# Kernel optimization log

Measured on AMD Instinct MI355X. Metric: run time of the kernel, lower is better.

The kernel has to match this reference:

```python
import jax, jax.numpy as jnp
import numpy as np
from jax import lax

# problem sizes and solver hyperparameters
B, N, G, T = 8, 128, 100, 24
N_ITERS, LR, RHO = 40, 2e-4, 10.0
VOLL, VOSP = 1000.0, 50.0
RES_UP, RES_DN, RT_UP, RT_DN, RAMP_F = 0.05, 0.02, 2.0, 0.5, 1.0


def setup_inputs() -> dict:
    k = jax.random.split(jax.random.key(0), 8)
    pmin = jax.random.uniform(k[0], (G,), minval=10.0, maxval=50.0)
    pmax = pmin + jax.random.uniform(k[1], (G,), minval=100.0, maxval=300.0)
    b_G = jax.random.uniform(k[2], (G,), minval=10.0, maxval=40.0)
    c_G = jax.random.uniform(k[3], (G,), minval=0.0, maxval=5.0)
    lo, hi = pmin.sum(), pmax.sum()
    forecast = lo + jax.random.uniform(k[4], (B, T)) * 0.5 * (hi - lo)
    omega_scen = 0.05 * hi * jax.random.normal(k[5], (B, N, T))
    om_min = omega_scen.min(axis=1) - 1.0
    om_max = omega_scen.max(axis=1) + 1.0
    eps = jax.random.uniform(k[6], (B,)) * 5.0
    return dict(forecast=forecast, omega_scen=omega_scen, om_min=om_min,
                om_max=om_max, eps=eps, pmin=pmin, pmax=pmax, b_G=b_G, c_G=c_G)


def _solve_one(forecast, omega, om_min, om_max, eps, pmin, pmax, b, c):
    # forecast [T], omega [N,T], om_min/om_max [T], eps scalar
    ramp = pmax * RAMP_F
    rup_p, rdn_p = RES_UP * b, RES_DN * b
    rtu_p, rtd_p = RT_UP * b, RT_DN * b
    dist_max = (om_max[None, :] - omega).sum(-1)   # [N]
    dist_min = (omega - om_min[None, :]).sum(-1)   # [N]

    def objective(v):
        Cost = b[:, None] * v['P'] + c[:, None]
        stage1 = (Cost.sum() + (rup_p[:, None] * v['R_up']).sum()
                  + (rdn_p[:, None] * v['R_dn']).sum())
        Qn = (jnp.einsum('g,ngt->n', rtu_p, v['d_up'])
              + jnp.einsum('g,ngt->n', rtd_p, v['d_dn'])
              + VOLL * v['LS'].sum(-1) + VOSP * v['SP'].sum(-1))
        Qmax = ((rtu_p[:, None] * v['du_max']).sum() + (rtd_p[:, None] * v['dd_max']).sum()
                + VOLL * v['LS_max'].sum() + VOSP * v['SP_max'].sum())
        Qmin = ((rtu_p[:, None] * v['du_min']).sum() + (rtd_p[:, None] * v['dd_min']).sum()
                + VOLL * v['LS_min'].sum() + VOSP * v['SP_min'].sum())
        # epigraph phi[n] >= Qn, >= Qmax - gamma*dist_max, >= Qmin - gamma*dist_min
        phi = jnp.maximum(Qn, jnp.maximum(Qmax - v['gamma'] * dist_max,
                                          Qmin - v['gamma'] * dist_min))
        obj = stage1 + phi.mean() + eps * v['gamma']
        return obj, (phi, Cost)

    def penalty(v):
        relu = jax.nn.relu
        dP = v['P'][:, 1:] - v['P'][:, :-1]
        res = [
            # equality constraints
            v['P'].sum(0) - forecast,
            (v['d_up'] - v['d_dn']).sum(1) + v['LS'] - v['SP'] - omega,
            (v['du_max'] - v['dd_max']).sum(0) + v['LS_max'] - v['SP_max'] - om_max,
            (v['du_min'] - v['dd_min']).sum(0) + v['LS_min'] - v['SP_min'] - om_min,
            # inequality constraints (relu of violation)
            relu(v['P'] + v['R_up'] - pmax[:, None]),
            relu(pmin[:, None] - (v['P'] - v['R_dn'])),
            relu(v['d_up'] - v['R_up'][None]),
            relu(v['d_dn'] - v['R_dn'][None]),
            relu(v['du_max'] - v['R_up']), relu(v['dd_max'] - v['R_dn']),
            relu(v['du_min'] - v['R_up']), relu(v['dd_min'] - v['R_dn']),
            relu(jnp.abs(dP) - ramp[:, None]),
        ]
        total = jnp.zeros(())
        for r in res:
            total = total + (r * r).sum()
        return total

    def loss(v):
        return objective(v)[0] + RHO * penalty(v)

    def project(v):
        v = {kk: jnp.maximum(vv, 0.0) for kk, vv in v.items()}
        v['P'] = jnp.clip(v['P'], pmin[:, None], pmax[:, None])
        return v

    z_gt = jnp.zeros((G, T))
    v0 = {'P': jnp.broadcast_to(0.5 * (pmin + pmax)[:, None], (G, T)),
          'R_up': z_gt, 'R_dn': z_gt,
          'd_up': jnp.zeros((N, G, T)), 'd_dn': jnp.zeros((N, G, T)),
          'LS': jnp.zeros((N, T)), 'SP': jnp.zeros((N, T)),
          'du_max': z_gt, 'dd_max': z_gt,
          'LS_max': jnp.zeros((T,)), 'SP_max': jnp.zeros((T,)),
          'du_min': z_gt, 'dd_min': z_gt,
          'LS_min': jnp.zeros((T,)), 'SP_min': jnp.zeros((T,)),
          'gamma': jnp.zeros(())}
    grad_fn = jax.grad(loss)

    def step(v, _):
        g = grad_fn(v)
        v = jax.tree_util.tree_map(lambda x, gx: x - LR * gx, v, g)
        return project(v), None

    v, _ = lax.scan(step, v0, None, length=N_ITERS)
    obj, (phi, Cost) = objective(v)
    return v['P'], v['R_up'], v['R_dn'], Cost, phi, v['gamma'], obj


def reference(forecast, omega_scen, om_min, om_max, eps, pmin, pmax, b_G, c_G):
    solve = jax.vmap(_solve_one, in_axes=(0, 0, 0, 0, 0, None, None, None, None))
    P, R_up, R_dn, Cost, phi, gamma, obj = solve(
        forecast, omega_scen, om_min, om_max, eps, pmin, pmax, b_G, c_G)
    return P, R_up, R_dn, Cost, phi, gamma, obj
```

## Files before the change

kernel.cpp:

```cpp
#include <hip/hip_runtime.h>
#include <hip/hip_cooperative_groups.h>

namespace cg = cooperative_groups;

#define G_ 100
#define T_ 24
#define NSC 128
#define BATCH 8
#define NITER 40
#define NBLK (BATCH*T_)
#define NTHR 512
#define GMAX 15

typedef unsigned long long u64;

__device__ __forceinline__ u64 gload64(const u64* p){
  return __hip_atomic_load(p, __ATOMIC_RELAXED, __HIP_MEMORY_SCOPE_AGENT);
}
__device__ __forceinline__ void gstore64(u64* p, u64 v){
  __hip_atomic_store(p, v, __ATOMIC_RELAXED, __HIP_MEMORY_SCOPE_AGENT);
}
__device__ __forceinline__ u64 pack(float v, unsigned tag){
  return ((u64)tag<<32) | (u64)__float_as_uint(v);
}
__device__ __forceinline__ float unpackv(u64 x){ return __uint_as_float((unsigned)x); }
__device__ __forceinline__ unsigned unpackt(u64 x){ return (unsigned)(x>>32); }

__device__ __forceinline__ void blockReduce2(float& a, float& b, float* sR){
#pragma unroll
  for (int off=32; off; off>>=1){ a+=__shfl_down(a,off,64); b+=__shfl_down(b,off,64); }
  const int w = threadIdx.x>>6;
  __syncthreads();
  if ((threadIdx.x&63)==0){ sR[w]=a; sR[8+w]=b; }
  __syncthreads();
  a=0.f; b=0.f;
#pragma unroll
  for (int i=0;i<8;++i){ a+=sR[i]; b+=sR[8+i]; }
}

__global__ __launch_bounds__(NTHR, 1) void dro_kernel(
    const float* __restrict__ forecast, const float* __restrict__ omega,
    const float* __restrict__ om_min, const float* __restrict__ om_max,
    const float* __restrict__ eps_in, const float* __restrict__ pmin_g,
    const float* __restrict__ pmax_g, const float* __restrict__ bG,
    const float* __restrict__ cG, float* __restrict__ out, float* __restrict__ ws)
{
  constexpr float LR=2e-4f, VOLL=1000.f, VOSP=50.f, TWO_RHO=20.f, INVN=1.f/128.f;
  const int blk=blockIdx.x;
  const int b=blk&7;
  const int t_own=blk>>3;
  const int tid=threadIdx.x, wave=tid>>6, lane=tid&63;
  int gbase, gcnt;
  if      (wave==0){ gbase=0;  gcnt=14; }
  else if (wave==1){ gbase=0;  gcnt=0;  }
  else if (wave==2){ gbase=14; gcnt=15; }
  else if (wave==3){ gbase=29; gcnt=15; }
  else             { gbase=44+(wave-4)*14; gcnt=14; }
  const bool pA = (wave!=1);

  __shared__ float sRu[2][G_], sRd[2][G_];
  __shared__ float sP[G_];
  __shared__ float sAccU[G_], sAccD[G_];
  __shared__ float sB[G_], sPmin[G_], sPmax[G_], sC[G_];
  __shared__ float sLS[NSC], sSP[NSC], sOm[NSC];
  __shared__ float sGQ[NSC], sR220[NSC];
  __shared__ float sQn[NSC], sDM[NSC], sDm[NSC], sS2[NSC];
  __shared__ float sQp[NSC*9], sSp[NSC*9];
  __shared__ float sQnP[NTHR];
  __shared__ float sRed[40];
  __shared__ float sScal[12];

  u64* W = (u64*)ws;
  u64* QNP = W;
  u64* PP  = W + 73728;
  u64* QS  = W + 147456;
  u64* GAM = W + 156672;
  u64* ST1 = W + 157056;

  const float epsv  = eps_in[b];
  const float omaxT = om_max[b*T_ + t_own];
  const float ominT = om_min[b*T_ + t_own];
  const float fctT  = forecast[b*T_ + t_own];

  float duA[GMAX], duB[GMAX], ddA[GMAX], ddB[GMAX];
  float duMr[2]={0.f,0.f}, ddMr[2]={0.f,0.f}, dumr[2]={0.f,0.f}, ddmr[2]={0.f,0.f};
  float lsm=0.f, spm=0.f, lsn=0.f, spn=0.f;
  float r3reg=0.f, r4reg=0.f, rPreg=0.f;

  if (tid<G_){
    sB[tid]=bG[tid]; sPmin[tid]=pmin_g[tid]; sPmax[tid]=pmax_g[tid]; sC[tid]=cG[tid];
    sRu[0][tid]=0.f; sRd[0][tid]=0.f;
    sAccU[tid]=0.f; sAccD[tid]=0.f;
  }
  if (tid<NSC){
    const int nn=tid;
    sLS[nn]=0.f; sSP[nn]=0.f; sS2[nn]=0.f;
    sOm[nn]=omega[(b*NSC+nn)*T_+t_own];
    float dM=0.f,dm=0.f;
    for (int t=0;t<T_;++t){
      float o=omega[(b*NSC+nn)*T_+t];
      dM+=om_max[b*T_+t]-o; dm+=o-om_min[b*T_+t];
    }
    sDM[nn]=dM; sDm[nn]=dm;
    sQp[nn*9+1]=0.f; sSp[nn*9+1]=0.f;
  }
  __syncthreads();
#pragma unroll
  for (int j=0;j<GMAX;++j){ duA[j]=0.f; duB[j]=0.f; ddA[j]=0.f; ddB[j]=0.f; }
  {
    float p0=0.f;
    if (tid<G_){
      p0=0.5f*(sPmin[tid]+sPmax[tid]);
      sP[tid]=p0;
      gstore64(&PP[b*3072 + t_own*128 + tid], pack(p0,1u));
    }
    if (tid<NSC) gstore64(&QNP[b*3072 + t_own*128 + tid], pack(0.f,1u));
    if (tid<2)   gstore64(&QS[(b*T_ + t_own)*16 + tid], pack(0.f,1u));
    if (t_own==0 && tid==0) gstore64(&GAM[b*16], pack(0.f,1u));
    float rp=p0, dum0=0.f;
    blockReduce2(rp,dum0,sRed);
    r3reg=-omaxT; r4reg=-ominT; rPreg=rp-fctT;
  }
  __syncthreads();

  for (int k=0;k<=NITER;++k){
    const unsigned tg  = (unsigned)(k+1);
    const unsigned tg2 = (unsigned)(k+2);
    const int rb = k%3, wb = (k+1)%3;
    const int kb = k&1, nbuf = kb^1;
    float* sRuC = sRu[kb];  float* sRdC = sRd[kb];
    float* sRuN = sRu[nbuf]; float* sRdN = sRd[nbuf];
    const u64* qnpR = QNP + rb*24576 + b*3072;
    const u64* ppR  = PP  + rb*24576 + b*3072;
    const u64* qsR  = QS  + (rb*BATCH + b)*T_*16;
    const u64* gamR = GAM + (rb*BATCH + b)*16;
    u64* qnpW = QNP + wb*24576 + b*3072 + t_own*128;
    u64* ppW  = PP  + wb*24576 + b*3072 + t_own*128;
    u64* qsW  = QS  + (wb*BATCH + b)*T_*16 + t_own*16;
    u64* gamW = GAM + (wb*BATCH + b)*16;

    const int n = tid&127, sb0 = (tid>>7)*6;
    const bool w0 = (wave==0), w1 = (wave==1), hasG1 = w1 && (lane<36);
    u64 xq[6];
#pragma unroll
    for (int s=0;s<6;++s) xq[s]=gload64(&qnpR[(sb0+s)*128+n]);
    u64 xm0=0,xm1=0,xp0=0,xp1=0,xs0=0,xs1=0,xg=0;
    if (w1){
      if (t_own>0){
        xm0=gload64(&ppR[(t_own-1)*128+lane]);
        if (hasG1) xm1=gload64(&ppR[(t_own-1)*128+lane+64]);
      }
      if (t_own<T_-1){
        xp0=gload64(&ppR[(t_own+1)*128+lane]);
        if (hasG1) xp1=gload64(&ppR[(t_own+1)*128+lane+64]);
      }
    } else if (w0){
      if (lane<T_){ xs0=gload64(&qsR[lane*16]); xs1=gload64(&qsR[lane*16+1]); }
      xg=gload64(gamR);
    }
    for (;;){
      bool pend=false;
#pragma unroll
      for (int s=0;s<6;++s)
        if (unpackt(xq[s])!=tg){ xq[s]=gload64(&qnpR[(sb0+s)*128+n]); pend=true; }
      if (w1){
        if (t_own>0){
          if (unpackt(xm0)!=tg){ xm0=gload64(&ppR[(t_own-1)*128+lane]); pend=true; }
          if (hasG1 && unpackt(xm1)!=tg){ xm1=gload64(&ppR[(t_own-1)*128+lane+64]); pend=true; }
        }
        if (t_own<T_-1){
          if (unpackt(xp0)!=tg){ xp0=gload64(&ppR[(t_own+1)*128+lane]); pend=true; }
          if (hasG1 && unpackt(xp1)!=tg){ xp1=gload64(&ppR[(t_own+1)*128+lane+64]); pend=true; }
        }
      } else if (w0){
        if (lane<T_){
          if (unpackt(xs0)!=tg){ xs0=gload64(&qsR[lane*16]);   pend=true; }
          if (unpackt(xs1)!=tg){ xs1=gload64(&qsR[lane*16+1]); pend=true; }
        }
        if (unpackt(xg)!=tg){ xg=gload64(gamR); pend=true; }
      }
      if (!pend) break;
      __builtin_amdgcn_s_sleep(1);
    }
    sQnP[tid]=unpackv(xq[0])+unpackv(xq[1])+unpackv(xq[2])
             +unpackv(xq[3])+unpackv(xq[4])+unpackv(xq[5]);
    float Qmax=unpackv(xs0), Qmin=unpackv(xs1);
    const float gamma=unpackv(xg);
    __syncthreads();

    if (k==NITER){
      if (w0){
#pragma unroll
        for (int off=32; off; off>>=1){ Qmax+=__shfl_xor(Qmax,off,64); Qmin+=__shfl_xor(Qmin,off,64); }
        if (lane==0){ sScal[2]=Qmax; sScal[3]=Qmin; sScal[4]=gamma; }
      }
      __syncthreads();
      const float Qm=sScal[2], Qn2=sScal[3], gam=sScal[4];
      if (tid<NSC){
        const float qsum=sQnP[tid]+sQnP[tid+128]+sQnP[tid+256]+sQnP[tid+384];
        const float ph=fmaxf(qsum,fmaxf(Qm-gam*sDM[tid],Qn2-gam*sDm[tid]));
        sQn[tid]=ph;
        if (t_own==0) out[76800 + b*NSC + tid]=ph;
      }
      float st=0.f, dum0=0.f;
      if (tid<G_){
        const int g=tid;
        const float Pv=sP[g];
        const float costv=sB[g]*Pv+sC[g];
        st=costv + 0.05f*sB[g]*sRuC[g] + 0.02f*sB[g]*sRdC[g];
        const int o=b*2400 + g*T_ + t_own;
        out[o]=Pv;
        out[19200+o]=sRuC[g];
        out[38400+o]=sRdC[g];
        out[57600+o]=costv;
      }
      blockReduce2(st,dum0,sRed);
      if (tid==0) gstore64(&ST1[(b*T_+t_own)*16], pack(st,99u));
      if (t_own==0){
        if (tid==0) out[77824+b]=gam;
        float s1=0.f;
        if (tid<64){
          u64 xs = (lane<T_)? gload64(&ST1[(b*T_+lane)*16]) : pack(0.f,99u);
          while (unpackt(xs)!=99u){ __builtin_amdgcn_s_sleep(1); xs=gload64(&ST1[(b*T_+lane)*16]); }
          s1=unpackv(xs);
        }
        float pm=(tid<NSC)? sQn[tid] : 0.f;
        blockReduce2(pm,s1,sRed);
        if (tid==0) out[77832+b] = s1 + pm*INVN + epsv*gam;
      }
      break;
    }

    if (w0){
#pragma unroll
      for (int off=32; off; off>>=1){ Qmax+=__shfl_xor(Qmax,off,64); Qmin+=__shfl_xor(Qmin,off,64); }
      float g1l=0.f,g2l=0.f,sgl=0.f;
#pragma unroll
      for (int h=0;h<2;++h){
        const int nn=lane+h*64;
        const float Qn=sQnP[nn]+sQnP[nn+128]+sQnP[nn+256]+sQnP[nn+384];
        const float m1=Qmax-gamma*sDM[nn], m2=Qmin-gamma*sDm[nn];
        const float inner=fmaxf(m1,m2), ph=fmaxf(Qn,inner);
        const float gQn=(Qn==ph?1.f:0.f)/((inner==ph)?2.f:1.f);
        const float gIn=(inner==ph?1.f:0.f)/((Qn==ph)?2.f:1.f);
        const float gm1=gIn*(m1==inner?1.f:0.f)/((m2==inner)?2.f:1.f);
        const float gm2=gIn*(m2==inner?1.f:0.f)/((m1==inner)?2.f:1.f);
        const float gq=gQn*INVN;
        sGQ[nn]=gq;
        g1l+=gm1; g2l+=gm2; sgl+=gm1*sDM[nn]+gm2*sDm[nn];
        const float r2=sS2[nn]+sLS[nn]-sSP[nn]-sOm[nn];
        const float r220=TWO_RHO*r2;
        sR220[nn]=r220;
        sLS[nn]=fmaxf(sLS[nn]-LR*(gq*VOLL+r220),0.f);
        sSP[nn]=fmaxf(sSP[nn]-LR*(gq*VOSP-r220),0.f);
      }
#pragma unroll
      for (int off=32; off; off>>=1){
        g1l+=__shfl_xor(g1l,off,64); g2l+=__shfl_xor(g2l,off,64); sgl+=__shfl_xor(sgl,off,64);
      }
      if (lane==0){ sScal[8]=g1l; sScal[9]=g2l; }
      if (t_own==0 && lane==0)
        gstore64(gamW, pack(fmaxf(gamma-LR*(epsv-INVN*sgl),0.f), tg2));
    }
    __syncthreads();

    if (pA){
      const float gqA=sGQ[lane],    r220A=sR220[lane];
      const float gqB=sGQ[lane+64], r220B=sR220[lane+64];
      float qvA=0.f,qvB=0.f,svA=0.f,svB=0.f;
#pragma unroll
      for (int j=0;j<GMAX;++j){
        if (j<gcnt){
          const int g=gbase+j;
          const float bg=sB[g];
          const float rtu=2.f*bg, rtd=0.5f*bg;
          const float ru=sRuC[g], rd=sRdC[g];
          const float r7A=fmaxf(duA[j]-ru,0.f), r8A=fmaxf(ddA[j]-rd,0.f);
          const float r7B=fmaxf(duB[j]-ru,0.f), r8B=fmaxf(ddB[j]-rd,0.f);
          duA[j]=fmaxf(duA[j]-LR*(gqA*rtu+(r220A+TWO_RHO*r7A)),0.f);
          ddA[j]=fmaxf(ddA[j]-LR*(gqA*rtd+(TWO_RHO*r8A-r220A)),0.f);
          duB[j]=fmaxf(duB[j]-LR*(gqB*rtu+(r220B+TWO_RHO*r7B)),0.f);
          ddB[j]=fmaxf(ddB[j]-LR*(gqB*rtd+(TWO_RHO*r8B-r220B)),0.f);
          qvA+=rtu*duA[j]+rtd*ddA[j];  svA+=duA[j]-ddA[j];
          qvB+=rtu*duB[j]+rtd*ddB[j];  svB+=duB[j]-ddB[j];
        }
      }
      sQp[lane*9+wave]=qvA;      sSp[lane*9+wave]=svA;
      sQp[(lane+64)*9+wave]=qvB; sSp[(lane+64)*9+wave]=svB;
    } else {
      const float r3=__shfl(r3reg,0,64), r4=__shfl(r4reg,0,64), rP=__shfl(rPreg,0,64);
      const float S1s=sScal[8], S2s=sScal[9];
      float pQx=0.f,pQn2=0.f,pr3=0.f,pr4=0.f,pP=0.f;
#pragma unroll
      for (int i=0;i<2;++i){
        if (i==0 || hasG1){
          const int g = lane + i*64;
          const float rupS=sAccU[g], rdnS=sAccD[g];
          const float Pold=sP[g], ru=sRuC[g], rd=sRdC[g];
          const float duMo=duMr[i], ddMo=ddMr[i], dumo=dumr[i], ddmo=ddmr[i];
          const float r5 =fmaxf(Pold+ru-sPmax[g],0.f);
          const float r6 =fmaxf(sPmin[g]-Pold+rd,0.f);
          const float r9 =fmaxf(duMo-ru,0.f), r10=fmaxf(ddMo-rd,0.f);
          const float r11=fmaxf(dumo-ru,0.f), r12=fmaxf(ddmo-rd,0.f);
          const float rampg=sPmax[g];
          float gP=sB[g]+TWO_RHO*(rP+r5-r6);
          if (t_own>0){
            const float dp=Pold-unpackv(i==0?xm0:xm1);
            gP+=TWO_RHO*fmaxf(fabsf(dp)-rampg,0.f)*(dp>=0.f?1.f:-1.f);
          }
          if (t_own<T_-1){
            const float dq=unpackv(i==0?xp0:xp1)-Pold;
            gP-=TWO_RHO*fmaxf(fabsf(dq)-rampg,0.f)*(dq>=0.f?1.f:-1.f);
          }
          const float Pn=fminf(fmaxf(Pold-LR*gP,sPmin[g]),sPmax[g]);
          sP[g]=Pn; gstore64(&ppW[g], pack(Pn,tg2));
          const float rtuB=2.f*sB[g], rtdB=0.5f*sB[g];
          sRuN[g]=fmaxf(ru-LR*(0.05f*sB[g]+TWO_RHO*(r5-rupS-r9-r11)),0.f);
          sRdN[g]=fmaxf(rd-LR*(0.02f*sB[g]+TWO_RHO*(r6-rdnS-r10-r12)),0.f);
          const float duMn=fmaxf(duMo-LR*(INVN*S1s*rtuB+TWO_RHO*( r3+r9 )),0.f);
          const float ddMn=fmaxf(ddMo-LR*(INVN*S1s*rtdB+TWO_RHO*(-r3+r10)),0.f);
          const float dumn=fmaxf(dumo-LR*(INVN*S2s*rtuB+TWO_RHO*( r4+r11)),0.f);
          const float ddmn=fmaxf(ddmo-LR*(INVN*S2s*rtdB+TWO_RHO*(-r4+r12)),0.f);
          duMr[i]=duMn; ddMr[i]=ddMn; dumr[i]=dumn; ddmr[i]=ddmn;
          pQx+=rtuB*duMn+rtdB*ddMn; pQn2+=rtuB*dumn+rtdB*ddmn;
          pr3+=duMn-ddMn; pr4+=dumn-ddmn; pP+=Pn;
        }
      }
#pragma unroll
      for (int off=32; off; off>>=1){
        pQx+=__shfl_down(pQx,off,64);  pQn2+=__shfl_down(pQn2,off,64);
        pr3+=__shfl_down(pr3,off,64);  pr4+=__shfl_down(pr4,off,64);
        pP +=__shfl_down(pP,off,64);
      }
      if (lane==0){
        const float LSMn=fmaxf(lsm-LR*(INVN*S1s*VOLL+TWO_RHO*r3),0.f);
        const float SPMn=fmaxf(spm-LR*(INVN*S1s*VOSP-TWO_RHO*r3),0.f);
        const float LSmn=fmaxf(lsn-LR*(INVN*S2s*VOLL+TWO_RHO*r4),0.f);
        const float SPmn=fmaxf(spn-LR*(INVN*S2s*VOSP-TWO_RHO*r4),0.f);
        lsm=LSMn; spm=SPMn; lsn=LSmn; spn=SPmn;
        gstore64(&qsW[0], pack(pQx + VOLL*LSMn + VOSP*SPMn, tg2));
        gstore64(&qsW[1], pack(pQn2 + VOLL*LSmn + VOSP*SPmn, tg2));
        r3reg=pr3 + LSMn - SPMn - omaxT;
        r4reg=pr4 + LSmn - SPmn - ominT;
        rPreg=pP - fctT;
      }
    }
    __syncthreads();

    if (tid>=256 && tid<384){
      const int nn=tid-256;
      float q=0.f,s=0.f;
#pragma unroll
      for (int w=0;w<8;++w){ q+=sQp[nn*9+w]; s+=sSp[nn*9+w]; }
      sS2[nn]=s;
      q += VOLL*sLS[nn]+VOSP*sSP[nn];
      gstore64(&qnpW[nn], pack(q,tg2));
    }
    if (pA){
#pragma unroll
      for (int j=0;j<GMAX;++j){
        if (j<gcnt){
          const int g=gbase+j;
          const float ru=sRuN[g], rd=sRdN[g];
          float aU=fmaxf(duA[j]-ru,0.f)+fmaxf(duB[j]-ru,0.f);
          float aD=fmaxf(ddA[j]-rd,0.f)+fmaxf(ddB[j]-rd,0.f);
#pragma unroll
          for (int off=32; off; off>>=1){ aU+=__shfl_xor(aU,off,64); aD+=__shfl_xor(aD,off,64); }
          if (lane==0){ sAccU[g]=aU; sAccD[g]=aD; }
        }
      }
    }
  }
}

extern "C" void kernel_launch(void* const* d_in, const int* in_sizes, int n_in,
                              void* d_out, int out_size, void* d_ws, size_t ws_size,
                              hipStream_t stream) {
  const float* forecast = (const float*)d_in[0];
  const float* omega    = (const float*)d_in[1];
  const float* omin     = (const float*)d_in[2];
  const float* omax     = (const float*)d_in[3];
  const float* eps      = (const float*)d_in[4];
  const float* pmin     = (const float*)d_in[5];
  const float* pmax     = (const float*)d_in[6];
  const float* bG       = (const float*)d_in[7];
  const float* cG       = (const float*)d_in[8];
  float* out = (float*)d_out;
  float* ws  = (float*)d_ws;
  void* args[] = { &forecast, &omega, &omin, &omax, &eps, &pmin, &pmax, &bG, &cG, &out, &ws };
  hipLaunchCooperativeKernel((const void*)dro_kernel, dim3(NBLK), dim3(NTHR),
                             args, 0, stream);
}
```

Measured before the change: 449.0 us.

## Replace per-element tag polling with per-block progress flags and rebalance generator waves

Each block now publishes one progress flag per iteration, after draining its stores and a block barrier. Wave 0 of each block polls the 24 flags of its batch before any data is loaded, so the per-element tag-check retry loops on the QNP/PP/QS/GAM buffers are removed. This is meant to cut repeated polling of many tagged 64-bit words, at the cost of an extra full store drain and barrier every iteration. Correctness now depends on the flag store being ordered after the data stores. The generator split across waves also changes: wave 0 takes 10 generators and waves 2–7 take 15 each, to even out per-wave work.

```diff
diff --git a/kernel.cpp b/kernel.cpp
--- a/kernel.cpp
+++ b/kernel.cpp
@@ -51,11 +51,9 @@
   const int t_own=blk>>3;
   const int tid=threadIdx.x, wave=tid>>6, lane=tid&63;
   int gbase, gcnt;
-  if      (wave==0){ gbase=0;  gcnt=14; }
+  if      (wave==0){ gbase=0;  gcnt=10; }
   else if (wave==1){ gbase=0;  gcnt=0;  }
-  else if (wave==2){ gbase=14; gcnt=15; }
-  else if (wave==3){ gbase=29; gcnt=15; }
-  else             { gbase=44+(wave-4)*14; gcnt=14; }
+  else             { gbase=10+(wave-2)*15; gcnt=15; }
   const bool pA = (wave!=1);
 
   __shared__ float sRu[2][G_], sRd[2][G_];
@@ -76,11 +74,14 @@
   u64* QS  = W + 147456;
   u64* GAM = W + 156672;
   u64* ST1 = W + 157056;
+  u64* FLG = W + 160128;
 
   const float epsv  = eps_in[b];
   const float omaxT = om_max[b*T_ + t_own];
   const float ominT = om_min[b*T_ + t_own];
   const float fctT  = forecast[b*T_ + t_own];
+  const u64* flB   = FLG + b*T_*16;
+  u64* myFlag      = FLG + (b*T_ + t_own)*16;
 
   float duA[GMAX], duB[GMAX], ddA[GMAX], ddB[GMAX];
   float duMr[2]={0.f,0.f}, ddMr[2]={0.f,0.f}, dumr[2]={0.f,0.f}, ddmr[2]={0.f,0.f};
@@ -121,11 +122,13 @@
     blockReduce2(rp,dum0,sRed);
     r3reg=-omaxT; r4reg=-ominT; rPreg=rp-fctT;
   }
+  __builtin_amdgcn_s_waitcnt(0);
   __syncthreads();
+  if (tid==0) gstore64(myFlag, 1ull);
 
   for (int k=0;k<=NITER;++k){
-    const unsigned tg  = (unsigned)(k+1);
     const unsigned tg2 = (unsigned)(k+2);
+    const u64 ftg = (u64)(k+1);
     const int rb = k%3, wb = (k+1)%3;
     const int kb = k&1, nbuf = kb^1;
     float* sRuC = sRu[kb];  float* sRdC = sRd[kb];
@@ -139,6 +142,15 @@
     u64* qsW  = QS  + (wb*BATCH + b)*T_*16 + t_own*16;
     u64* gamW = GAM + (wb*BATCH + b)*16;
 
+    if (tid < 64){
+      for (;;){
+        u64 f = (lane < T_) ? gload64(&flB[lane*16]) : ftg;
+        if (__ballot(f < ftg) == 0ull) break;
+        __builtin_amdgcn_s_sleep(1);
+      }
+    }
+    __syncthreads();
+
     const int n = tid&127, sb0 = (tid>>7)*6;
     const bool w0 = (wave==0), w1 = (wave==1), hasG1 = w1 && (lane<36);
     u64 xq[6];
@@ -157,30 +169,6 @@
     } else if (w0){
       if (lane<T_){ xs0=gload64(&qsR[lane*16]); xs1=gload64(&qsR[lane*16+1]); }
       xg=gload64(gamR);
-    }
-    for (;;){
-      bool pend=false;
-#pragma unroll
-      for (int s=0;s<6;++s)
-        if (unpackt(xq[s])!=tg){ xq[s]=gload64(&qnpR[(sb0+s)*128+n]); pend=true; }
-      if (w1){
-        if (t_own>0){
-          if (unpackt(xm0)!=tg){ xm0=gload64(&ppR[(t_own-1)*128+lane]); pend=true; }
-          if (hasG1 && unpackt(xm1)!=tg){ xm1=gload64(&ppR[(t_own-1)*128+lane+64]); pend=true; }
-        }
-        if (t_own<T_-1){
-          if (unpackt(xp0)!=tg){ xp0=gload64(&ppR[(t_own+1)*128+lane]); pend=true; }
-          if (hasG1 && unpackt(xp1)!=tg){ xp1=gload64(&ppR[(t_own+1)*128+lane+64]); pend=true; }
-        }
-      } else if (w0){
-        if (lane<T_){
-          if (unpackt(xs0)!=tg){ xs0=gload64(&qsR[lane*16]);   pend=true; }
-          if (unpackt(xs1)!=tg){ xs1=gload64(&qsR[lane*16+1]); pend=true; }
-        }
-        if (unpackt(xg)!=tg){ xg=gload64(gamR); pend=true; }
-      }
-      if (!pend) break;
-      __builtin_amdgcn_s_sleep(1);
     }
     sQnP[tid]=unpackv(xq[0])+unpackv(xq[1])+unpackv(xq[2])
              +unpackv(xq[3])+unpackv(xq[4])+unpackv(xq[5]);
@@ -356,6 +344,11 @@
       q += VOLL*sLS[nn]+VOSP*sSP[nn];
       gstore64(&qnpW[nn], pack(q,tg2));
     }
+
+    __builtin_amdgcn_s_waitcnt(0);
+    __syncthreads();
+    if (tid==0) gstore64(myFlag, (u64)(k+2));
+
     if (pA){
 #pragma unroll
       for (int j=0;j<GMAX;++j){
```

New measurement: 490.1 us. 9.1% more time.
